# Optimization experiments

Hardware: AMD Instinct MI355X
Metric: run time of the kernel (lower is better)

Reference implementation:

```python
import jax, jax.numpy as jnp
import numpy as np

B, T, C = 4, 4096, 256

def setup_inputs() -> dict:
    key = jax.random.key(0)
    kx, km, kk, kq, kv = jax.random.split(key, 5)
    x = jax.random.normal(kx, (B, T, C), dtype=jnp.float32)
    mask = jax.random.randint(km, (B, T), 0, 2, dtype=jnp.int32)
    s = C ** -0.5
    Wk = jax.random.normal(kk, (C, C), dtype=jnp.float32) * s
    Wq = jax.random.normal(kq, (C, C), dtype=jnp.float32) * s
    Wv = jax.random.normal(kv, (C, C), dtype=jnp.float32) * s
    return {"x": x, "mask": mask, "Wk": Wk, "Wq": Wq, "Wv": Wv}

def reference(x, mask, Wk, Wq, Wv):
    # nn.Linear: y = x @ W.T  (W is [out, in])
    k = jnp.einsum('btc,dc->btd', x, Wk)   # [B,T,C]
    q = jnp.einsum('btc,dc->btd', x, Wq)   # [B,T,C]
    v = jnp.einsum('btc,dc->btd', x, Wv)   # [B,T,C]
    scale = k.shape[-1] ** -0.5
    weights = jnp.einsum('bqc,bkc->bqk', q, k) * scale  # [B,T,T]
    # torch quirk: mask.float().masked_fill(mask==0, -inf) adds +1.0 where mask!=0
    mask_f = jnp.where(mask == 0, -jnp.inf, mask.astype(weights.dtype))  # [B,T]
    masked = weights + mask_f[:, None, :]   # broadcast over query dim == repeat(1,T,1)
    attn = jax.nn.softmax(masked, axis=-1)
    out = jnp.einsum('bqk,bkc->bqc', attn, v)  # [B,T,C]
    return out
```

## Files before the change

kernel.cpp:

```cpp
#include <hip/hip_runtime.h>


typedef __attribute__((ext_vector_type(8)))  _Float16 f16x8;
typedef __attribute__((ext_vector_type(4)))  _Float16 f16x4;
typedef __attribute__((ext_vector_type(4)))  float    f32x4;
typedef __attribute__((ext_vector_type(16))) float    f32x16;

constexpr int Bb = 4;
constexpr int Tt = 4096;
constexpr int Cc = 256;
constexpr int BT = Bb * Tt;
constexpr int NI = 64;

#define MFMA16(a, b, c) __builtin_amdgcn_mfma_f32_16x16x32_f16((a), (b), (c), 0, 0, 0)
#define MFMA32(a, b, c) __builtin_amdgcn_mfma_f32_32x32x16_f16((a), (b), (c), 0, 0, 0)

__device__ __forceinline__ void gl16(const _Float16* gp, char* lp) {
    __builtin_amdgcn_global_load_lds(
        (const __attribute__((address_space(1))) void*)gp,
        (__attribute__((address_space(3))) void*)lp, 16, 0, 0);
}

__global__ __launch_bounds__(256) void qkv_proj(
    const float* __restrict__ x,
    const float* __restrict__ Wq, const float* __restrict__ Wk,
    const float* __restrict__ Wv,
    _Float16* __restrict__ qo, _Float16* __restrict__ ko,
    _Float16* __restrict__ vto)
{
    extern __shared__ _Float16 sm[];
    _Float16* xs = sm;
    _Float16* wsm = sm + 128 * 264;

    const int tid = threadIdx.x;
    const int m0  = blockIdx.x * 128;
    const int ny  = blockIdx.y;
    const int mat = ny >> 1;
    const int d0  = (ny & 1) * 128;
    const float* W = (mat == 0) ? Wq : (mat == 1 ? Wk : Wv);

#pragma unroll
    for (int i = 0; i < 32; ++i) {
        int flat = i * 256 + tid;
        int r = flat >> 6, c4 = (flat & 63) << 2;
        float4 v = *reinterpret_cast<const float4*>(x + (size_t)(m0 + r) * Cc + c4);
        f16x4 h = { (_Float16)v.x, (_Float16)v.y, (_Float16)v.z, (_Float16)v.w };
        *reinterpret_cast<f16x4*>(xs + r * 264 + c4) = h;
    }
#pragma unroll
    for (int i = 0; i < 32; ++i) {
        int flat = i * 256 + tid;
        int r = flat >> 6, c4 = (flat & 63) << 2;
        float4 v = *reinterpret_cast<const float4*>(W + (size_t)(d0 + r) * Cc + c4);
        f16x4 h = { (_Float16)v.x, (_Float16)v.y, (_Float16)v.z, (_Float16)v.w };
        *reinterpret_cast<f16x4*>(wsm + r * 264 + c4) = h;
    }
    __syncthreads();

    const int w = tid >> 6, lane = tid & 63;
    const int lr = lane & 15, lg = lane >> 4;

    f32x4 acc[2][8] = {};

#pragma unroll
    for (int kc = 0; kc < 8; ++kc) {
        const int c0 = kc * 32 + lg * 8;
        f16x8 xf[2], wf[8];
#pragma unroll
        for (int mb = 0; mb < 2; ++mb)
            xf[mb] = *reinterpret_cast<const f16x8*>(xs + (w * 32 + mb * 16 + lr) * 264 + c0);
#pragma unroll
        for (int db = 0; db < 8; ++db)
            wf[db] = *reinterpret_cast<const f16x8*>(wsm + (db * 16 + lr) * 264 + c0);
        if (mat != 2) {
#pragma unroll
            for (int mb = 0; mb < 2; ++mb)
#pragma unroll
                for (int db = 0; db < 8; ++db)
                    acc[mb][db] = MFMA16(wf[db], xf[mb], acc[mb][db]);
        } else {
#pragma unroll
            for (int mb = 0; mb < 2; ++mb)
#pragma unroll
                for (int db = 0; db < 8; ++db)
                    acc[mb][db] = MFMA16(xf[mb], wf[db], acc[mb][db]);
        }
    }

    if (mat != 2) {
        const float sc = (mat == 0) ? 0.0625f : 1.0f;
        const int jj  = (lg & 1) * 4;
#pragma unroll
        for (int mb = 0; mb < 2; ++mb)
#pragma unroll
            for (int db = 0; db < 8; ++db) {
                int m  = m0 + w * 32 + mb * 16 + lr;
                int c  = d0 + db * 16 + lg * 4;
                int kc = c >> 5;
                int ch = (c >> 3) & 3;
                f32x4 a = acc[mb][db];
                f16x4 h = { (_Float16)(a.x * sc), (_Float16)(a.y * sc),
                            (_Float16)(a.z * sc), (_Float16)(a.w * sc) };
                if (mat == 0) {
                    size_t off = (size_t)(m >> 5) * 8192 + (((m >> 4) & 1) * 8 + kc) * 512
                               + ch * 128 + (m & 15) * 8 + jj;
                    *reinterpret_cast<f16x4*>(qo + off) = h;
                } else {
                    size_t off = (size_t)(m >> 4) * 4096 + kc * 512
                               + ch * 128 + (m & 15) * 8 + jj;
                    *reinterpret_cast<f16x4*>(ko + off) = h;
                }
            }
    } else {
        const int jj = (lg & 1) * 4;
        const int kh = (lg >> 1) & 1;
#pragma unroll
        for (int mb = 0; mb < 2; ++mb)
#pragma unroll
            for (int db = 0; db < 8; ++db) {
                int d = d0 + db * 16 + lr;
                int m = m0 + w * 32 + mb * 16 + lg * 4;
                f32x4 a = acc[mb][db];
                f16x4 h = { (_Float16)a.x, (_Float16)a.y, (_Float16)a.z, (_Float16)a.w };
                size_t off = (size_t)(m >> 4) * 4096 + (d >> 5) * 512
                           + kh * 256 + (d & 31) * 8 + jj;
                *reinterpret_cast<f16x4*>(vto + off) = h;
            }
    }
}

__global__ __launch_bounds__(512, 2) void attn_kernel(
    const _Float16* __restrict__ qb, const _Float16* __restrict__ kb,
    const _Float16* __restrict__ vtb, const int* __restrict__ mask,
    float* __restrict__ outp)
{
    extern __shared__ char smraw[];
    float* mex32 = (float*)(smraw + 143360);
    float* lex32 = (float*)(smraw + 144384);
    float* oexf  = (float*)smraw;

    const int tid = threadIdx.x, w = tid >> 6, lane = tid & 63;
    const int qw = w >> 2, g = w & 3;
    const int l15 = lane & 15, l4 = lane >> 4;
    const int l31 = lane & 31, l5 = lane >> 5;

    const int bid = blockIdx.x;
    const int b   = (bid & 7) >> 1;
    const int qt  = ((bid >> 3) << 1) | (bid & 1);
    const int q0  = qt * 64;
    const size_t base = (size_t)b * Tt * Cc;
    const int* maskb = mask + (size_t)b * Tt;
    const _Float16* kTb = kb + base;
    const _Float16* vTb = vtb + base;

    f16x8 qf[2][8];
    {
        const _Float16* qTb = qb + (size_t)(b * 128 + qt * 2 + qw) * 8192;
#pragma unroll
        for (int qh = 0; qh < 2; ++qh)
#pragma unroll
            for (int kc = 0; kc < 8; ++kc)
                qf[qh][kc] = *reinterpret_cast<const f16x8*>(
                    qTb + (qh * 8 + kc) * 512 + l4 * 128 + l15 * 8);
    }

    _Float16* pw = (_Float16*)(smraw + 131072) + w * 768;

    f32x16 o[8] = {};
    float m0r = -60.f, m1r = -60.f, l0r = 0.f, l1r = 0.f;

    auto STAGE = [&](int i, int buf) {
        const int kt = i * 4 + g;
        char* dst = smraw + buf * 65536 + g * 16384 + (qw ? 8192 : 0);
        const _Float16* src = (qw ? vTb : kTb) + (size_t)kt * 4096 + lane * 8;
#pragma unroll
        for (int j = 0; j < 8; ++j)
            gl16(src + j * 512, dst + j * 1024);
    };

    STAGE(0, 0);
    asm volatile("s_waitcnt vmcnt(0)" ::: "memory");

    int cur = 0;
#pragma unroll 1
    for (int i = 0; i < NI; ++i) {
        __syncthreads();
        if (i + 1 < NI) STAGE(i + 1, cur ^ 1);

        const _Float16* kb_ = (const _Float16*)(smraw + cur * 65536 + g * 16384);
        const _Float16* vb_ = kb_ + 4096;
        int4 mc = *reinterpret_cast<const int4*>(maskb + (i * 4 + g) * 16 + l4 * 4);

        f32x4 s40 = { 0.f, 0.f, 0.f, 0.f }, s41 = { 0.f, 0.f, 0.f, 0.f };
        __builtin_amdgcn_s_setprio(1);
#pragma unroll
        for (int kc = 0; kc < 8; ++kc) {
            f16x8 kf = *reinterpret_cast<const f16x8*>(kb_ + kc * 512 + l4 * 128 + l15 * 8);
            s40 = MFMA16(kf, qf[0][kc], s40);
            s41 = MFMA16(kf, qf[1][kc], s41);
        }
        __builtin_amdgcn_s_setprio(0);

        if (mc.x == 0) { s40[0] = -1e30f; s41[0] = -1e30f; }
        if (mc.y == 0) { s40[1] = -1e30f; s41[1] = -1e30f; }
        if (mc.z == 0) { s40[2] = -1e30f; s41[2] = -1e30f; }
        if (mc.w == 0) { s40[3] = -1e30f; s41[3] = -1e30f; }

        float t0 = fmaxf(fmaxf(s40[0], s40[1]), fmaxf(s40[2], s40[3]));
        float t1 = fmaxf(fmaxf(s41[0], s41[1]), fmaxf(s41[2], s41[3]));
        t0 = fmaxf(t0, __shfl_xor(t0, 16, 64)); t0 = fmaxf(t0, __shfl_xor(t0, 32, 64));
        t1 = fmaxf(t1, __shfl_xor(t1, 16, 64)); t1 = fmaxf(t1, __shfl_xor(t1, 32, 64));

        if (__any(t0 > m0r + 8.f || t1 > m1r + 8.f)) {
            float mn0 = fmaxf(m0r, t0), mn1 = fmaxf(m1r, t1);
            float c0 = __expf(m0r - mn0), c1 = __expf(m1r - mn1);
            m0r = mn0; m1r = mn1; l0r *= c0; l1r *= c1;
            float cs = (lane & 16) ? c1 : c0;
#pragma unroll
            for (int dt = 0; dt < 8; ++dt) o[dt] *= cs;
        }

        float rs0 = 0.f, rs1 = 0.f;
#pragma unroll
        for (int r = 0; r < 4; ++r) {
            float p0 = __expf(s40[r] - m0r); s40[r] = p0; rs0 += p0;
            float p1 = __expf(s41[r] - m1r); s41[r] = p1; rs1 += p1;
        }
        rs0 += __shfl_xor(rs0, 16, 64); rs0 += __shfl_xor(rs0, 32, 64);
        rs1 += __shfl_xor(rs1, 16, 64); rs1 += __shfl_xor(rs1, 32, 64);
        l0r += rs0; l1r += rs1;

        {
            f16x4 h0 = { (_Float16)s40[0], (_Float16)s40[1], (_Float16)s40[2], (_Float16)s40[3] };
            f16x4 h1 = { (_Float16)s41[0], (_Float16)s41[1], (_Float16)s41[2], (_Float16)s41[3] };
            *reinterpret_cast<f16x4*>(pw + l15 * 24 + l4 * 4)        = h0;
            *reinterpret_cast<f16x4*>(pw + (16 + l15) * 24 + l4 * 4) = h1;
        }
        f16x8 pf = *reinterpret_cast<const f16x8*>(pw + l31 * 24 + l5 * 8);

        __builtin_amdgcn_s_setprio(1);
#pragma unroll
        for (int dt = 0; dt < 8; ++dt) {
            f16x8 vf = *reinterpret_cast<const f16x8*>(vb_ + dt * 512 + l5 * 256 + l31 * 8);
            o[dt] = MFMA32(vf, pf, o[dt]);
        }
        __builtin_amdgcn_s_setprio(0);

        asm volatile("s_waitcnt vmcnt(0)" ::: "memory");
        cur ^= 1;
    }
    __syncthreads();

    if (l4 == 0) {
        mex32[(qw * 4 + g) * 32 + l15]      = m0r;
        mex32[(qw * 4 + g) * 32 + 16 + l15] = m1r;
        lex32[(qw * 4 + g) * 32 + l15]      = l0r;
        lex32[(qw * 4 + g) * 32 + 16 + l15] = l1r;
    }
    __syncthreads();

    float mq = (lane & 16) ? m1r : m0r;
    float mst = -1e30f;
#pragma unroll
    for (int g2 = 0; g2 < 4; ++g2)
        mst = fmaxf(mst, mex32[(qw * 4 + g2) * 32 + l31]);
    float osc = __expf(mq - mst);

#pragma unroll 1
    for (int s = 0; s < 2; ++s) {
        if (qw == s) {
            float* og = oexf + g * (32 * 258);
#pragma unroll
            for (int dt = 0; dt < 8; ++dt)
#pragma unroll
                for (int r = 0; r < 16; ++r) {
                    int d = dt * 32 + (r & 3) + 8 * (r >> 2) + 4 * l5;
                    og[l31 * 258 + d] = o[dt][r] * osc;
                }
        }
        __syncthreads();
        {
            const int q = tid >> 4, dg = tid & 15;
            float mA = mex32[(s * 4 + 0) * 32 + q], mB = mex32[(s * 4 + 1) * 32 + q];
            float mC = mex32[(s * 4 + 2) * 32 + q], mD = mex32[(s * 4 + 3) * 32 + q];
            float ms = fmaxf(fmaxf(mA, mB), fmaxf(mC, mD));
            float lt = lex32[(s * 4 + 0) * 32 + q] * __expf(mA - ms)
                     + lex32[(s * 4 + 1) * 32 + q] * __expf(mB - ms)
                     + lex32[(s * 4 + 2) * 32 + q] * __expf(mC - ms)
                     + lex32[(s * 4 + 3) * 32 + q] * __expf(mD - ms);
            float inv = 1.f / lt;
#pragma unroll
            for (int i = 0; i < 4; ++i) {
                int d0 = dg * 16 + i * 4;
                f32x4 a = *reinterpret_cast<const f32x4*>(oexf + q * 258 + d0);
#pragma unroll
                for (int g2 = 1; g2 < 4; ++g2) {
                    f32x4 t = *reinterpret_cast<const f32x4*>(
                        oexf + g2 * (32 * 258) + q * 258 + d0);
                    a[0] += t[0]; a[1] += t[1]; a[2] += t[2]; a[3] += t[3];
                }
                a[0] *= inv; a[1] *= inv; a[2] *= inv; a[3] *= inv;
                *reinterpret_cast<f32x4*>(
                    outp + base + (size_t)(q0 + s * 32 + q) * Cc + d0) = a;
            }
        }
        __syncthreads();
    }
}

extern "C" void kernel_launch(void* const* d_in, const int* in_sizes, int n_in,
                              void* d_out, int out_size, void* d_ws, size_t ws_size,
                              hipStream_t stream)
{
    (void)in_sizes; (void)n_in; (void)out_size; (void)ws_size;
    const float* x   = (const float*)d_in[0];
    const int*  mask = (const int*)d_in[1];
    const float* Wk  = (const float*)d_in[2];
    const float* Wq  = (const float*)d_in[3];
    const float* Wv  = (const float*)d_in[4];
    float* out = (float*)d_out;

    _Float16* q  = (_Float16*)d_ws;
    _Float16* k  = q + (size_t)BT * Cc;
    _Float16* vt = k + (size_t)BT * Cc;

    dim3 gA(128, 6), blkA(256);
    size_t ldsA = (size_t)(128 + 128) * 264 * sizeof(_Float16);
    qkv_proj<<<gA, blkA, ldsA, stream>>>(x, Wq, Wk, Wv, q, k, vt);

    dim3 gB(256), blkB(512);
    size_t ldsB = 145408;
    attn_kernel<<<gB, blkB, ldsB, stream>>>(q, k, vt, mask, out);
}
```

Baseline: 138.5 us.

## Give each wave private K/V LDS tiles and drop per-iteration block barriers

Each wave now owns private K and V staging buffers in LDS and loads its own contiguous range of key tiles, so the per-iteration __syncthreads is removed. K for the next tile is prefetched right after the QK MFMAs and V after the PV MFMAs, ordered with fine-grained vmcnt/lgkmcnt waits, and the mask load is prefetched one iteration ahead. The two per-row running maxima are merged into one shared max per wave, which shrinks the shuffle reductions but couples both query halves' rescaling. This risks fp16 underflow when rows have very different maxima, and relies on exact vmcnt counting for correctness.

```diff
diff --git a/kernel.cpp b/kernel.cpp
--- a/kernel.cpp
+++ b/kernel.cpp
@@ -164,58 +164,67 @@
                     qTb + (qh * 8 + kc) * 512 + l4 * 128 + l15 * 8);
     }
 
+    char* kbase = smraw + w * 16384;
+    char* vbase = kbase + 8192;
+    const _Float16* kbL = (const _Float16*)kbase;
+    const _Float16* vbL = (const _Float16*)vbase;
     _Float16* pw = (_Float16*)(smraw + 131072) + w * 768;
 
     f32x16 o[8] = {};
-    float m0r = -60.f, m1r = -60.f, l0r = 0.f, l1r = 0.f;
-
-    auto STAGE = [&](int i, int buf) {
-        const int kt = i * 4 + g;
-        char* dst = smraw + buf * 65536 + g * 16384 + (qw ? 8192 : 0);
-        const _Float16* src = (qw ? vTb : kTb) + (size_t)kt * 4096 + lane * 8;
-#pragma unroll
-        for (int j = 0; j < 8; ++j)
-            gl16(src + j * 512, dst + j * 1024);
+    float m_run = -60.f, l0r = 0.f, l1r = 0.f;
+
+    auto STAGE_K = [&](int i) {
+        const _Float16* src = kTb + (size_t)(g * 64 + i) * 4096 + lane * 8;
+#pragma unroll
+        for (int j = 0; j < 8; ++j) gl16(src + j * 512, kbase + j * 1024);
     };
-
-    STAGE(0, 0);
-    asm volatile("s_waitcnt vmcnt(0)" ::: "memory");
-
-    int cur = 0;
+    auto STAGE_V = [&](int i) {
+        const _Float16* src = vTb + (size_t)(g * 64 + i) * 4096 + lane * 8;
+#pragma unroll
+        for (int j = 0; j < 8; ++j) gl16(src + j * 512, vbase + j * 1024);
+    };
+
+    int4 mcur = *reinterpret_cast<const int4*>(maskb + (g * 64) * 16 + l4 * 4);
+    STAGE_K(0);
+    STAGE_V(0);
+
 #pragma unroll 1
     for (int i = 0; i < NI; ++i) {
-        __syncthreads();
-        if (i + 1 < NI) STAGE(i + 1, cur ^ 1);
-
-        const _Float16* kb_ = (const _Float16*)(smraw + cur * 65536 + g * 16384);
-        const _Float16* vb_ = kb_ + 4096;
-        int4 mc = *reinterpret_cast<const int4*>(maskb + (i * 4 + g) * 16 + l4 * 4);
+        asm volatile("s_waitcnt vmcnt(8)" ::: "memory");
 
         f32x4 s40 = { 0.f, 0.f, 0.f, 0.f }, s41 = { 0.f, 0.f, 0.f, 0.f };
         __builtin_amdgcn_s_setprio(1);
 #pragma unroll
         for (int kc = 0; kc < 8; ++kc) {
-            f16x8 kf = *reinterpret_cast<const f16x8*>(kb_ + kc * 512 + l4 * 128 + l15 * 8);
+            f16x8 kf = *reinterpret_cast<const f16x8*>(kbL + kc * 512 + l4 * 128 + l15 * 8);
             s40 = MFMA16(kf, qf[0][kc], s40);
             s41 = MFMA16(kf, qf[1][kc], s41);
         }
         __builtin_amdgcn_s_setprio(0);
 
-        if (mc.x == 0) { s40[0] = -1e30f; s41[0] = -1e30f; }
-        if (mc.y == 0) { s40[1] = -1e30f; s41[1] = -1e30f; }
-        if (mc.z == 0) { s40[2] = -1e30f; s41[2] = -1e30f; }
-        if (mc.w == 0) { s40[3] = -1e30f; s41[3] = -1e30f; }
+        asm volatile("s_waitcnt lgkmcnt(0)" ::: "memory");
+        int4 mnext = mcur;
+        if (i + 1 < NI) {
+            mnext = *reinterpret_cast<const int4*>(
+                maskb + (g * 64 + i + 1) * 16 + l4 * 4);
+            STAGE_K(i + 1);
+        }
+
+        if (mcur.x == 0) { s40[0] = -1e30f; s41[0] = -1e30f; }
+        if (mcur.y == 0) { s40[1] = -1e30f; s41[1] = -1e30f; }
+        if (mcur.z == 0) { s40[2] = -1e30f; s41[2] = -1e30f; }
+        if (mcur.w == 0) { s40[3] = -1e30f; s41[3] = -1e30f; }
 
         float t0 = fmaxf(fmaxf(s40[0], s40[1]), fmaxf(s40[2], s40[3]));
         float t1 = fmaxf(fmaxf(s41[0], s41[1]), fmaxf(s41[2], s41[3]));
-        t0 = fmaxf(t0, __shfl_xor(t0, 16, 64)); t0 = fmaxf(t0, __shfl_xor(t0, 32, 64));
-        t1 = fmaxf(t1, __shfl_xor(t1, 16, 64)); t1 = fmaxf(t1, __shfl_xor(t1, 32, 64));
-
-        if (__any(t0 > m0r + 8.f || t1 > m1r + 8.f)) {
-            float mn0 = fmaxf(m0r, t0), mn1 = fmaxf(m1r, t1);
-            float c0 = __expf(m0r - mn0), c1 = __expf(m1r - mn1);
-            m0r = mn0; m1r = mn1; l0r *= c0; l1r *= c1;
-            float cs = (lane & 16) ? c1 : c0;
+        float tm = fmaxf(t0, t1);
+        tm = fmaxf(tm, __shfl_xor(tm, 16, 64));
+        tm = fmaxf(tm, __shfl_xor(tm, 32, 64));
+
+        if (__any(tm > m_run + 8.f)) {
+            float mn = fmaxf(m_run, tm);
+            float cs = __expf(m_run - mn);
+            m_run = mn; l0r *= cs; l1r *= cs;
 #pragma unroll
             for (int dt = 0; dt < 8; ++dt) o[dt] *= cs;
         }
@@ -223,8 +232,8 @@
         float rs0 = 0.f, rs1 = 0.f;
 #pragma unroll
         for (int r = 0; r < 4; ++r) {
-            float p0 = __expf(s40[r] - m0r); s40[r] = p0; rs0 += p0;
-            float p1 = __expf(s41[r] - m1r); s41[r] = p1; rs1 += p1;
+            float p0 = __expf(s40[r] - m_run); s40[r] = p0; rs0 += p0;
+            float p1 = __expf(s41[r] - m_run); s41[r] = p1; rs1 += p1;
         }
         rs0 += __shfl_xor(rs0, 16, 64); rs0 += __shfl_xor(rs0, 32, 64);
         rs1 += __shfl_xor(rs1, 16, 64); rs1 += __shfl_xor(rs1, 32, 64);
@@ -238,33 +247,36 @@
         }
         f16x8 pf = *reinterpret_cast<const f16x8*>(pw + l31 * 24 + l5 * 8);
 
+        if (i + 1 < NI) asm volatile("s_waitcnt vmcnt(9)" ::: "memory");
+        else            asm volatile("s_waitcnt vmcnt(0)" ::: "memory");
+
         __builtin_amdgcn_s_setprio(1);
 #pragma unroll
         for (int dt = 0; dt < 8; ++dt) {
-            f16x8 vf = *reinterpret_cast<const f16x8*>(vb_ + dt * 512 + l5 * 256 + l31 * 8);
+            f16x8 vf = *reinterpret_cast<const f16x8*>(vbL + dt * 512 + l5 * 256 + l31 * 8);
             o[dt] = MFMA32(vf, pf, o[dt]);
         }
         __builtin_amdgcn_s_setprio(0);
 
-        asm volatile("s_waitcnt vmcnt(0)" ::: "memory");
-        cur ^= 1;
+        asm volatile("s_waitcnt lgkmcnt(0)" ::: "memory");
+        if (i + 1 < NI) STAGE_V(i + 1);
+        mcur = mnext;
     }
     __syncthreads();
 
     if (l4 == 0) {
-        mex32[(qw * 4 + g) * 32 + l15]      = m0r;
-        mex32[(qw * 4 + g) * 32 + 16 + l15] = m1r;
+        mex32[(qw * 4 + g) * 32 + l15]      = m_run;
+        mex32[(qw * 4 + g) * 32 + 16 + l15] = m_run;
         lex32[(qw * 4 + g) * 32 + l15]      = l0r;
         lex32[(qw * 4 + g) * 32 + 16 + l15] = l1r;
     }
     __syncthreads();
 
-    float mq = (lane & 16) ? m1r : m0r;
     float mst = -1e30f;
 #pragma unroll
     for (int g2 = 0; g2 < 4; ++g2)
         mst = fmaxf(mst, mex32[(qw * 4 + g2) * 32 + l31]);
-    float osc = __expf(mq - mst);
+    float osc = __expf(m_run - mst);
 
 #pragma unroll 1
     for (int s = 0; s < 2; ++s) {
```

New measurement: 149.6 us. +8.0%, slower.

## Process two key tiles per softmax step and switch to exp2 with prescaled queries

Applied to the files above, without the earlier changes.

The attention loop now computes scores for two consecutive 16-key tiles before doing one softmax update and one PV accumulation over 32 keys. This halves the max/sum reductions, rescale checks and P stores per key. K and V staging are split: one query-wave group streams K every iteration, the other loads V two tiles at a time. Queries are prescaled by log2(e) so exp2f replaces __expf. LDS use grows to hold the split buffers and the wider P tile, which may reduce occupancy headroom. It also changes the load balance between the two wave groups.

```diff
diff --git a/kernel.cpp b/kernel.cpp
--- a/kernel.cpp
+++ b/kernel.cpp
@@ -10,7 +10,7 @@
 constexpr int Tt = 4096;
 constexpr int Cc = 256;
 constexpr int BT = Bb * Tt;
-constexpr int NI = 64;
+constexpr int NT = 64;
 
 #define MFMA16(a, b, c) __builtin_amdgcn_mfma_f32_16x16x32_f16((a), (b), (c), 0, 0, 0)
 #define MFMA32(a, b, c) __builtin_amdgcn_mfma_f32_32x32x16_f16((a), (b), (c), 0, 0, 0)
@@ -88,7 +88,7 @@
     }
 
     if (mat != 2) {
-        const float sc = (mat == 0) ? 0.0625f : 1.0f;
+        const float sc = (mat == 0) ? 0.0625f * 1.44269504f : 1.0f;
         const int jj  = (lg & 1) * 4;
 #pragma unroll
         for (int mb = 0; mb < 2; ++mb)
@@ -135,8 +135,8 @@
     float* __restrict__ outp)
 {
     extern __shared__ char smraw[];
-    float* mex32 = (float*)(smraw + 143360);
-    float* lex32 = (float*)(smraw + 144384);
+    float* mex32 = (float*)(smraw + 151552);
+    float* lex32 = (float*)(smraw + 152576);
     float* oexf  = (float*)smraw;
 
     const int tid = threadIdx.x, w = tid >> 6, lane = tid & 63;
@@ -164,90 +164,117 @@
                     qTb + (qh * 8 + kc) * 512 + l4 * 128 + l15 * 8);
     }
 
-    _Float16* pw = (_Float16*)(smraw + 131072) + w * 768;
+    char* kreg = smraw + g * 16384;
+    char* vreg = smraw + 65536 + g * 16384;
+    _Float16* pw = (_Float16*)(smraw + 131072) + w * 1280;
 
     f32x16 o[8] = {};
     float m0r = -60.f, m1r = -60.f, l0r = 0.f, l1r = 0.f;
 
-    auto STAGE = [&](int i, int buf) {
-        const int kt = i * 4 + g;
-        char* dst = smraw + buf * 65536 + g * 16384 + (qw ? 8192 : 0);
-        const _Float16* src = (qw ? vTb : kTb) + (size_t)kt * 4096 + lane * 8;
-#pragma unroll
-        for (int j = 0; j < 8; ++j)
-            gl16(src + j * 512, dst + j * 1024);
+    auto STAGE_K = [&](int t) {
+        char* dst = kreg + (t & 1) * 8192;
+        const _Float16* src = kTb + (size_t)(t * 4 + g) * 4096 + lane * 8;
+#pragma unroll
+        for (int j = 0; j < 8; ++j) gl16(src + j * 512, dst + j * 1024);
     };
-
-    STAGE(0, 0);
+    auto STAGE_V = [&](int t) {
+        char* dst = vreg + (t & 1) * 8192;
+        const _Float16* src = vTb + (size_t)(t * 4 + g) * 4096 + lane * 8;
+#pragma unroll
+        for (int j = 0; j < 8; ++j) gl16(src + j * 512, dst + j * 1024);
+    };
+
+    if (qw == 0) STAGE_K(0);
     asm volatile("s_waitcnt vmcnt(0)" ::: "memory");
 
-    int cur = 0;
+    f32x4 s00, s01, s10, s11;
+
 #pragma unroll 1
-    for (int i = 0; i < NI; ++i) {
+    for (int t = 0; t < NT; ++t) {
         __syncthreads();
-        if (i + 1 < NI) STAGE(i + 1, cur ^ 1);
-
-        const _Float16* kb_ = (const _Float16*)(smraw + cur * 65536 + g * 16384);
-        const _Float16* vb_ = kb_ + 4096;
-        int4 mc = *reinterpret_cast<const int4*>(maskb + (i * 4 + g) * 16 + l4 * 4);
-
-        f32x4 s40 = { 0.f, 0.f, 0.f, 0.f }, s41 = { 0.f, 0.f, 0.f, 0.f };
+        if (qw == 0) { if (t + 1 < NT) STAGE_K(t + 1); }
+        else if (!(t & 1)) { STAGE_V(t); if (t + 1 < NT) STAGE_V(t + 1); }
+
+        const _Float16* kb_ = (const _Float16*)(kreg + (t & 1) * 8192);
+        int4 mc = *reinterpret_cast<const int4*>(maskb + (t * 4 + g) * 16 + l4 * 4);
+
+        f32x4 sa = { 0.f, 0.f, 0.f, 0.f }, sb = { 0.f, 0.f, 0.f, 0.f };
         __builtin_amdgcn_s_setprio(1);
 #pragma unroll
         for (int kc = 0; kc < 8; ++kc) {
             f16x8 kf = *reinterpret_cast<const f16x8*>(kb_ + kc * 512 + l4 * 128 + l15 * 8);
-            s40 = MFMA16(kf, qf[0][kc], s40);
-            s41 = MFMA16(kf, qf[1][kc], s41);
+            sa = MFMA16(kf, qf[0][kc], sa);
+            sb = MFMA16(kf, qf[1][kc], sb);
         }
         __builtin_amdgcn_s_setprio(0);
 
-        if (mc.x == 0) { s40[0] = -1e30f; s41[0] = -1e30f; }
-        if (mc.y == 0) { s40[1] = -1e30f; s41[1] = -1e30f; }
-        if (mc.z == 0) { s40[2] = -1e30f; s41[2] = -1e30f; }
-        if (mc.w == 0) { s40[3] = -1e30f; s41[3] = -1e30f; }
-
-        float t0 = fmaxf(fmaxf(s40[0], s40[1]), fmaxf(s40[2], s40[3]));
-        float t1 = fmaxf(fmaxf(s41[0], s41[1]), fmaxf(s41[2], s41[3]));
-        t0 = fmaxf(t0, __shfl_xor(t0, 16, 64)); t0 = fmaxf(t0, __shfl_xor(t0, 32, 64));
-        t1 = fmaxf(t1, __shfl_xor(t1, 16, 64)); t1 = fmaxf(t1, __shfl_xor(t1, 32, 64));
-
-        if (__any(t0 > m0r + 8.f || t1 > m1r + 8.f)) {
-            float mn0 = fmaxf(m0r, t0), mn1 = fmaxf(m1r, t1);
-            float c0 = __expf(m0r - mn0), c1 = __expf(m1r - mn1);
-            m0r = mn0; m1r = mn1; l0r *= c0; l1r *= c1;
-            float cs = (lane & 16) ? c1 : c0;
-#pragma unroll
-            for (int dt = 0; dt < 8; ++dt) o[dt] *= cs;
-        }
-
-        float rs0 = 0.f, rs1 = 0.f;
-#pragma unroll
-        for (int r = 0; r < 4; ++r) {
-            float p0 = __expf(s40[r] - m0r); s40[r] = p0; rs0 += p0;
-            float p1 = __expf(s41[r] - m1r); s41[r] = p1; rs1 += p1;
-        }
-        rs0 += __shfl_xor(rs0, 16, 64); rs0 += __shfl_xor(rs0, 32, 64);
-        rs1 += __shfl_xor(rs1, 16, 64); rs1 += __shfl_xor(rs1, 32, 64);
-        l0r += rs0; l1r += rs1;
-
-        {
-            f16x4 h0 = { (_Float16)s40[0], (_Float16)s40[1], (_Float16)s40[2], (_Float16)s40[3] };
-            f16x4 h1 = { (_Float16)s41[0], (_Float16)s41[1], (_Float16)s41[2], (_Float16)s41[3] };
-            *reinterpret_cast<f16x4*>(pw + l15 * 24 + l4 * 4)        = h0;
-            *reinterpret_cast<f16x4*>(pw + (16 + l15) * 24 + l4 * 4) = h1;
-        }
-        f16x8 pf = *reinterpret_cast<const f16x8*>(pw + l31 * 24 + l5 * 8);
-
-        __builtin_amdgcn_s_setprio(1);
-#pragma unroll
-        for (int dt = 0; dt < 8; ++dt) {
-            f16x8 vf = *reinterpret_cast<const f16x8*>(vb_ + dt * 512 + l5 * 256 + l31 * 8);
-            o[dt] = MFMA32(vf, pf, o[dt]);
-        }
-        __builtin_amdgcn_s_setprio(0);
+        if (mc.x == 0) { sa[0] = -1e30f; sb[0] = -1e30f; }
+        if (mc.y == 0) { sa[1] = -1e30f; sb[1] = -1e30f; }
+        if (mc.z == 0) { sa[2] = -1e30f; sb[2] = -1e30f; }
+        if (mc.w == 0) { sa[3] = -1e30f; sb[3] = -1e30f; }
+
+        if (!(t & 1)) {
+            s00 = sa; s01 = sb;
+        } else {
+            s10 = sa; s11 = sb;
+
+            float t0 = fmaxf(fmaxf(fmaxf(s00[0], s00[1]), fmaxf(s00[2], s00[3])),
+                             fmaxf(fmaxf(s10[0], s10[1]), fmaxf(s10[2], s10[3])));
+            float t1 = fmaxf(fmaxf(fmaxf(s01[0], s01[1]), fmaxf(s01[2], s01[3])),
+                             fmaxf(fmaxf(s11[0], s11[1]), fmaxf(s11[2], s11[3])));
+            t0 = fmaxf(t0, __shfl_xor(t0, 16, 64)); t0 = fmaxf(t0, __shfl_xor(t0, 32, 64));
+            t1 = fmaxf(t1, __shfl_xor(t1, 16, 64)); t1 = fmaxf(t1, __shfl_xor(t1, 32, 64));
+
+            if (__any(t0 > m0r + 11.54f || t1 > m1r + 11.54f)) {
+                float mn0 = fmaxf(m0r, t0), mn1 = fmaxf(m1r, t1);
+                float c0 = exp2f(m0r - mn0), c1 = exp2f(m1r - mn1);
+                m0r = mn0; m1r = mn1; l0r *= c0; l1r *= c1;
+                float cs = (lane & 16) ? c1 : c0;
+#pragma unroll
+                for (int dt = 0; dt < 8; ++dt) o[dt] *= cs;
+            }
+
+            float rs0 = 0.f, rs1 = 0.f;
+#pragma unroll
+            for (int r = 0; r < 4; ++r) {
+                float p;
+                p = exp2f(s00[r] - m0r); s00[r] = p; rs0 += p;
+                p = exp2f(s10[r] - m0r); s10[r] = p; rs0 += p;
+                p = exp2f(s01[r] - m1r); s01[r] = p; rs1 += p;
+                p = exp2f(s11[r] - m1r); s11[r] = p; rs1 += p;
+            }
+            rs0 += __shfl_xor(rs0, 16, 64); rs0 += __shfl_xor(rs0, 32, 64);
+            rs1 += __shfl_xor(rs1, 16, 64); rs1 += __shfl_xor(rs1, 32, 64);
+            l0r += rs0; l1r += rs1;
+
+            {
+                f16x4 h;
+                h = (f16x4){ (_Float16)s00[0], (_Float16)s00[1], (_Float16)s00[2], (_Float16)s00[3] };
+                *reinterpret_cast<f16x4*>(pw + l15 * 40 + l4 * 4) = h;
+                h = (f16x4){ (_Float16)s10[0], (_Float16)s10[1], (_Float16)s10[2], (_Float16)s10[3] };
+                *reinterpret_cast<f16x4*>(pw + l15 * 40 + 16 + l4 * 4) = h;
+                h = (f16x4){ (_Float16)s01[0], (_Float16)s01[1], (_Float16)s01[2], (_Float16)s01[3] };
+                *reinterpret_cast<f16x4*>(pw + (16 + l15) * 40 + l4 * 4) = h;
+                h = (f16x4){ (_Float16)s11[0], (_Float16)s11[1], (_Float16)s11[2], (_Float16)s11[3] };
+                *reinterpret_cast<f16x4*>(pw + (16 + l15) * 40 + 16 + l4 * 4) = h;
+            }
+            f16x8 pf0 = *reinterpret_cast<const f16x8*>(pw + l31 * 40 + l5 * 8);
+            f16x8 pf1 = *reinterpret_cast<const f16x8*>(pw + l31 * 40 + 16 + l5 * 8);
+
+            __builtin_amdgcn_s_setprio(1);
+#pragma unroll
+            for (int dt = 0; dt < 8; ++dt) {
+                f16x8 vf0 = *reinterpret_cast<const f16x8*>(
+                    vreg + 0 * 8192 + dt * 1024 + l5 * 512 + l31 * 16);
+                o[dt] = MFMA32(vf0, pf0, o[dt]);
+                f16x8 vf1 = *reinterpret_cast<const f16x8*>(
+                    vreg + 1 * 8192 + dt * 1024 + l5 * 512 + l31 * 16);
+                o[dt] = MFMA32(vf1, pf1, o[dt]);
+            }
+            __builtin_amdgcn_s_setprio(0);
+        }
 
         asm volatile("s_waitcnt vmcnt(0)" ::: "memory");
-        cur ^= 1;
     }
     __syncthreads();
 
@@ -264,7 +291,7 @@
 #pragma unroll
     for (int g2 = 0; g2 < 4; ++g2)
         mst = fmaxf(mst, mex32[(qw * 4 + g2) * 32 + l31]);
-    float osc = __expf(mq - mst);
+    float osc = exp2f(mq - mst);
 
 #pragma unroll 1
     for (int s = 0; s < 2; ++s) {
@@ -284,10 +311,10 @@
             float mA = mex32[(s * 4 + 0) * 32 + q], mB = mex32[(s * 4 + 1) * 32 + q];
             float mC = mex32[(s * 4 + 2) * 32 + q], mD = mex32[(s * 4 + 3) * 32 + q];
             float ms = fmaxf(fmaxf(mA, mB), fmaxf(mC, mD));
-            float lt = lex32[(s * 4 + 0) * 32 + q] * __expf(mA - ms)
-                     + lex32[(s * 4 + 1) * 32 + q] * __expf(mB - ms)
-                     + lex32[(s * 4 + 2) * 32 + q] * __expf(mC - ms)
-                     + lex32[(s * 4 + 3) * 32 + q] * __expf(mD - ms);
+            float lt = lex32[(s * 4 + 0) * 32 + q] * exp2f(mA - ms)
+                     + lex32[(s * 4 + 1) * 32 + q] * exp2f(mB - ms)
+                     + lex32[(s * 4 + 2) * 32 + q] * exp2f(mC - ms)
+                     + lex32[(s * 4 + 3) * 32 + q] * exp2f(mD - ms);
             float inv = 1.f / lt;
 #pragma unroll
             for (int i = 0; i < 4; ++i) {
@@ -295,9 +322,9 @@
                 f32x4 a = *reinterpret_cast<const f32x4*>(oexf + q * 258 + d0);
 #pragma unroll
                 for (int g2 = 1; g2 < 4; ++g2) {
-                    f32x4 t = *reinterpret_cast<const f32x4*>(
+                    f32x4 tt = *reinterpret_cast<const f32x4*>(
                         oexf + g2 * (32 * 258) + q * 258 + d0);
-                    a[0] += t[0]; a[1] += t[1]; a[2] += t[2]; a[3] += t[3];
+                    a[0] += tt[0]; a[1] += tt[1]; a[2] += tt[2]; a[3] += tt[3];
                 }
                 a[0] *= inv; a[1] *= inv; a[2] *= inv; a[3] *= inv;
                 *reinterpret_cast<f32x4*>(
@@ -329,6 +356,6 @@
     qkv_proj<<<gA, blkA, ldsA, stream>>>(x, Wq, Wk, Wv, q, k, vt);
 
     dim3 gB(256), blkB(512);
-    size_t ldsB = 145408;
+    size_t ldsB = 153600;
     attn_kernel<<<gB, blkB, ldsB, stream>>>(q, k, vt, mask, out);
 }
```

Result: slower. 145.6 us (+5.1%).
